# Optimization experiments

Hardware: AMD Instinct MI355X
Metric: run time of the kernel (lower is better)

## Reference

```python
import jax, jax.numpy as jnp
import numpy as np

EMBEDDING_DIM = 64  # matches init_kwargs; temperature = sqrt(embedding_dim)


def setup_inputs() -> dict:
    key = jax.random.key(0)
    k1, k2, k3, k4 = jax.random.split(key, 4)
    B, S, D = 8, 2048, EMBEDDING_DIM
    return {
        "key": jax.random.normal(k1, (B, S, D), dtype=jnp.float32),
        "query": jax.random.normal(k2, (B, S, D), dtype=jnp.float32),
        "value": jax.random.normal(k3, (B, S, D), dtype=jnp.float32),
        "query_attention_mask": jax.random.randint(k4, (B, S), 0, 2, dtype=jnp.int32),
    }


def reference(key, query, value, query_attention_mask):
    # scores: [B, S, S]
    temperature = jnp.sqrt(jnp.asarray(EMBEDDING_DIM, dtype=query.dtype))
    scores = jnp.einsum("bqd,bkd->bqk", query, key) / temperature
    # masked_fill_ fills -inf WHERE mask is True (as in the torch source).
    # mask [B, S] -> broadcast over the query axis to [B, 1, S] -> [B, S, S].
    mask = query_attention_mask.astype(bool)[:, None, :]
    scores = jnp.where(mask, -jnp.inf, scores)
    attention_filter = jax.nn.softmax(scores, axis=-1)
    # dropout p=0.0 (deterministic reference) -> identity
    context = jnp.einsum("bqk,bkd->bqd", attention_filter, value)
    return (context, attention_filter)
```

## Files before the change

### kernel.cpp

```cpp
#include <hip/hip_runtime.h>
#include <hip/hip_bf16.h>
#include <math.h>


typedef short bf16x8 __attribute__((ext_vector_type(8)));
typedef short bf16x4 __attribute__((ext_vector_type(4)));
typedef float f32x4 __attribute__((ext_vector_type(4)));

#define BATCH 8
#define SDIM 2048
#define DDIM 64
#define KBLK 64
#define NBLK (SDIM / KBLK)
#define KSPLIT 4
#define BPW (NBLK / KSPLIT)
#define NROWS (BATCH * SDIM)
#define SCALE 0.125f
#define KSTR 72

__device__ __forceinline__ short f2bf(float f) {
    unsigned x = __float_as_uint(f);
    x = (x + 0x7fffu + ((x >> 16) & 1u)) >> 16;
    return (short)x;
}
__device__ __forceinline__ float fidx(const float4& v, int i) {
    return ((const float*)&v)[i];
}

__global__ __launch_bounds__(256, 4)
void attn_prep(const float* __restrict__ Kg, const float* __restrict__ Vg,
               short* __restrict__ Kbf, short* __restrict__ VTbf,
               float* __restrict__ Ctx)
{
    __shared__ short VTlds[DDIM][KSTR];

    const int wg = blockIdx.x;
    const int b = wg & 7;
    const int kbase = (wg >> 3) * KBLK;
    const int tid = threadIdx.x;

    const float* Kb = Kg + (size_t)b * SDIM * DDIM;
    const float* Vb = Vg + (size_t)b * SDIM * DDIM;

    {
        const int key = tid >> 2, doff = (tid & 3) * 16;
        const float* src = Kb + (size_t)(kbase + key) * DDIM + doff;
        float4 f0 = *(const float4*)(src);
        float4 f1 = *(const float4*)(src + 4);
        float4 f2 = *(const float4*)(src + 8);
        float4 f3 = *(const float4*)(src + 12);
        bf16x8 p0, p1;
        p0[0]=f2bf(f0.x); p0[1]=f2bf(f0.y); p0[2]=f2bf(f0.z); p0[3]=f2bf(f0.w);
        p0[4]=f2bf(f1.x); p0[5]=f2bf(f1.y); p0[6]=f2bf(f1.z); p0[7]=f2bf(f1.w);
        p1[0]=f2bf(f2.x); p1[1]=f2bf(f2.y); p1[2]=f2bf(f2.z); p1[3]=f2bf(f2.w);
        p1[4]=f2bf(f3.x); p1[5]=f2bf(f3.y); p1[6]=f2bf(f3.z); p1[7]=f2bf(f3.w);
        short* dst = Kbf + ((size_t)b * SDIM + kbase + key) * DDIM + doff;
        *(bf16x8*)dst = p0;
        *(bf16x8*)(dst + 8) = p1;
    }

    {
        const int sv_d0 = (tid & 15) * 4, sv_k0 = (tid >> 4) * 4;
        float4 vreg[4];
        #pragma unroll
        for (int i = 0; i < 4; ++i)
            vreg[i] = *(const float4*)(Vb + (size_t)(kbase + sv_k0 + i) * DDIM + sv_d0);
        #pragma unroll
        for (int dd = 0; dd < 4; ++dd) {
            bf16x4 pv;
            pv[0] = f2bf(fidx(vreg[0], dd));
            pv[1] = f2bf(fidx(vreg[1], dd));
            pv[2] = f2bf(fidx(vreg[2], dd));
            pv[3] = f2bf(fidx(vreg[3], dd));
            *(bf16x4*)&VTlds[sv_d0 + dd][sv_k0] = pv;
        }
    }
    __syncthreads();
    {
        const int d = tid >> 2, koff = (tid & 3) * 16;
        bf16x8 a = *(const bf16x8*)&VTlds[d][koff];
        bf16x8 c = *(const bf16x8*)&VTlds[d][koff + 8];
        short* dst = VTbf + ((size_t)b * DDIM + d) * SDIM + kbase + koff;
        *(bf16x8*)dst = a;
        *(bf16x8*)(dst + 8) = c;
    }

    {
        float4* dst = (float4*)Ctx + (size_t)wg * 1024;
        for (int i = tid; i < 1024; i += 256) dst[i] = make_float4(0.f, 0.f, 0.f, 0.f);
    }
}

__global__ __launch_bounds__(256, 4)
void attn_stats(const short* __restrict__ Kbf, const float* __restrict__ Qg,
                const int* __restrict__ Mg, float* __restrict__ part)
{
    __shared__ short Klds[KBLK][KSTR];
    __shared__ int   Mlds[KBLK];

    const int wg = blockIdx.x;
    const int b = wg & 7;
    const int qt = (wg >> 3) & 31;
    const int sp = wg >> 8;
    const int tid = threadIdx.x;
    const int w = tid >> 6, lane = tid & 63, col = lane & 15, quad = lane >> 4;

    const float* Qb = Qg + (size_t)b * SDIM * DDIM;
    const int*   Mb = Mg + (size_t)b * SDIM;

    bf16x8 aq[2];
    {
        const float* qsrc = Qb + (size_t)(qt * 64 + w * 16 + col) * DDIM + quad * 8;
        #pragma unroll
        for (int c = 0; c < 2; ++c) {
            float4 f0 = *(const float4*)(qsrc + c * 32);
            float4 f1 = *(const float4*)(qsrc + c * 32 + 4);
            bf16x8 a;
            a[0]=f2bf(f0.x); a[1]=f2bf(f0.y); a[2]=f2bf(f0.z); a[3]=f2bf(f0.w);
            a[4]=f2bf(f1.x); a[5]=f2bf(f1.y); a[6]=f2bf(f1.z); a[7]=f2bf(f1.w);
            aq[c] = a;
        }
    }

    const int skey = tid >> 2;
    const int sdoff = (tid & 3) * 16;
    const int kb0 = sp * BPW * KBLK;
    const short* Ksp = Kbf + ((size_t)b * SDIM + kb0) * DDIM;

    float lsum[4];
    #pragma unroll
    for (int r = 0; r < 4; ++r) lsum[r] = 0.0f;

    bf16x8 ks0, ks1;
    int mreg = 0;
    {
        const short* src = Ksp + (size_t)skey * DDIM + sdoff;
        ks0 = *(const bf16x8*)src;
        ks1 = *(const bf16x8*)(src + 8);
        if (tid < KBLK) mreg = Mb[kb0 + tid];
    }

    for (int kb = 0; kb < BPW; ++kb) {
        __syncthreads();
        *(bf16x8*)&Klds[skey][sdoff]     = ks0;
        *(bf16x8*)&Klds[skey][sdoff + 8] = ks1;
        if (tid < KBLK) Mlds[tid] = mreg;
        __syncthreads();
        if (kb + 1 < BPW) {
            const short* src = Ksp + (size_t)((kb + 1) * KBLK + skey) * DDIM + sdoff;
            ks0 = *(const bf16x8*)src;
            ks1 = *(const bf16x8*)(src + 8);
            if (tid < KBLK) mreg = Mb[kb0 + (kb + 1) * KBLK + tid];
        }

        #pragma unroll
        for (int t = 0; t < 4; ++t) {
            f32x4 acc = {0.f, 0.f, 0.f, 0.f};
            #pragma unroll
            for (int c = 0; c < 2; ++c) {
                bf16x8 bk = *(const bf16x8*)&Klds[t * 16 + col][c * 32 + quad * 8];
                acc = __builtin_amdgcn_mfma_f32_16x16x32_bf16(aq[c], bk, acc, 0, 0, 0);
            }
            const int mk = Mlds[t * 16 + col];
            #pragma unroll
            for (int r = 0; r < 4; ++r)
                lsum[r] += mk ? 0.0f : __expf(acc[r] * SCALE);
        }
    }

    #pragma unroll
    for (int r = 0; r < 4; ++r) {
        float s = lsum[r];
        s += __shfl_xor(s, 1);
        s += __shfl_xor(s, 2);
        s += __shfl_xor(s, 4);
        s += __shfl_xor(s, 8);
        lsum[r] = s;
    }
    if (col == 0) {
        #pragma unroll
        for (int r = 0; r < 4; ++r)
            part[(size_t)sp * NROWS + b * SDIM + qt * 64 + w * 16 + quad * 4 + r] = lsum[r];
    }
}

__global__ __launch_bounds__(256)
void attn_merge(const float* __restrict__ part, float* __restrict__ stats)
{
    const int t = blockIdx.x * 256 + threadIdx.x;
    if (t < NROWS) {
        float l = part[t] + part[NROWS + t] + part[2 * NROWS + t] + part[3 * NROWS + t];
        stats[t] = 1.0f / l;
    }
}

__global__ __launch_bounds__(256, 4)
void attn_emit(const short* __restrict__ Kbf, const short* __restrict__ VTbf,
               const float* __restrict__ Qg, const int* __restrict__ Mg,
               const float* __restrict__ stats, float* __restrict__ Ctx,
               float* __restrict__ Filt)
{
    __shared__ short Klds[KBLK][KSTR];
    __shared__ short VTlds[DDIM][KSTR];
    __shared__ short Plds[4][16][KSTR];
    __shared__ int   Mlds[KBLK];

    const int wg = blockIdx.x;
    const int b = wg & 7;
    const int qt = (wg >> 3) & 31;
    const int sp = wg >> 8;
    const int tid = threadIdx.x;
    const int w = tid >> 6, lane = tid & 63, col = lane & 15, quad = lane >> 4;

    const float* Qb = Qg + (size_t)b * SDIM * DDIM;
    const int*   Mb = Mg + (size_t)b * SDIM;
    float* Ctxb  = Ctx  + (size_t)b * SDIM * DDIM;
    float* Filtb = Filt + (size_t)b * SDIM * SDIM;

    bf16x8 aq[2];
    {
        const float* qsrc = Qb + (size_t)(qt * 64 + w * 16 + col) * DDIM + quad * 8;
        #pragma unroll
        for (int c = 0; c < 2; ++c) {
            float4 f0 = *(const float4*)(qsrc + c * 32);
            float4 f1 = *(const float4*)(qsrc + c * 32 + 4);
            bf16x8 a;
            a[0]=f2bf(f0.x); a[1]=f2bf(f0.y); a[2]=f2bf(f0.z); a[3]=f2bf(f0.w);
            a[4]=f2bf(f1.x); a[5]=f2bf(f1.y); a[6]=f2bf(f1.z); a[7]=f2bf(f1.w);
            aq[c] = a;
        }
    }

    float invl[4];
    #pragma unroll
    for (int r = 0; r < 4; ++r)
        invl[r] = stats[b * SDIM + qt * 64 + w * 16 + quad * 4 + r];

    const int skey = tid >> 2;
    const int sdoff = (tid & 3) * 16;
    const int kb0 = sp * BPW * KBLK;
    const short* Ksp = Kbf + ((size_t)b * SDIM + kb0) * DDIM;
    const short* VTb = VTbf + (size_t)b * DDIM * SDIM;
    const int vd = tid >> 2, vkoff = (tid & 3) * 16;

    f32x4 Oacc[4];
    #pragma unroll
    for (int dt = 0; dt < 4; ++dt) Oacc[dt] = (f32x4){0.f, 0.f, 0.f, 0.f};

    bf16x8 ks0, ks1, vt0, vt1;
    int mreg = 0;
    {
        const short* srck = Ksp + (size_t)skey * DDIM + sdoff;
        ks0 = *(const bf16x8*)srck;
        ks1 = *(const bf16x8*)(srck + 8);
        const short* srcv = VTb + (size_t)vd * SDIM + kb0 + vkoff;
        vt0 = *(const bf16x8*)srcv;
        vt1 = *(const bf16x8*)(srcv + 8);
        if (tid < KBLK) mreg = Mb[kb0 + tid];
    }

    for (int kb = 0; kb < BPW; ++kb) {
        const int kbase = kb0 + kb * KBLK;
        __syncthreads();
        *(bf16x8*)&Klds[skey][sdoff]      = ks0;
        *(bf16x8*)&Klds[skey][sdoff + 8]  = ks1;
        *(bf16x8*)&VTlds[vd][vkoff]       = vt0;
        *(bf16x8*)&VTlds[vd][vkoff + 8]   = vt1;
        if (tid < KBLK) Mlds[tid] = mreg;
        __syncthreads();
        if (kb + 1 < BPW) {
            const short* srck = Ksp + (size_t)((kb + 1) * KBLK + skey) * DDIM + sdoff;
            ks0 = *(const bf16x8*)srck;
            ks1 = *(const bf16x8*)(srck + 8);
            const short* srcv = VTb + (size_t)vd * SDIM + (kbase + KBLK) + vkoff;
            vt0 = *(const bf16x8*)srcv;
            vt1 = *(const bf16x8*)(srcv + 8);
            if (tid < KBLK) mreg = Mb[kbase + KBLK + tid];
        }

        #pragma unroll
        for (int t = 0; t < 4; ++t) {
            f32x4 acc = {0.f, 0.f, 0.f, 0.f};
            #pragma unroll
            for (int c = 0; c < 2; ++c) {
                bf16x8 bk = *(const bf16x8*)&Klds[t * 16 + col][c * 32 + quad * 8];
                acc = __builtin_amdgcn_mfma_f32_16x16x32_bf16(aq[c], bk, acc, 0, 0, 0);
            }
            const int mk = Mlds[t * 16 + col];
            #pragma unroll
            for (int r = 0; r < 4; ++r) {
                float p = mk ? 0.0f : __expf(acc[r] * SCALE) * invl[r];
                __builtin_nontemporal_store(
                    p, &Filtb[(size_t)(qt * 64 + w * 16 + quad * 4 + r) * SDIM + kbase + t * 16 + col]);
                Plds[w][quad * 4 + r][t * 16 + col] = f2bf(p);
            }
        }

        #pragma unroll
        for (int c = 0; c < 2; ++c) {
            bf16x8 ap = *(const bf16x8*)&Plds[w][col][c * 32 + quad * 8];
            #pragma unroll
            for (int dt = 0; dt < 4; ++dt) {
                bf16x8 bv = *(const bf16x8*)&VTlds[dt * 16 + col][c * 32 + quad * 8];
                Oacc[dt] = __builtin_amdgcn_mfma_f32_16x16x32_bf16(ap, bv, Oacc[dt], 0, 0, 0);
            }
        }
    }

    #pragma unroll
    for (int dt = 0; dt < 4; ++dt) {
        #pragma unroll
        for (int r = 0; r < 4; ++r) {
            unsafeAtomicAdd(&Ctxb[(size_t)(qt * 64 + w * 16 + quad * 4 + r) * DDIM + dt * 16 + col],
                            Oacc[dt][r]);
        }
    }
}

extern "C" void kernel_launch(void* const* d_in, const int* in_sizes, int n_in,
                              void* d_out, int out_size, void* d_ws, size_t ws_size,
                              hipStream_t stream) {
    const float* Kg = (const float*)d_in[0];
    const float* Qg = (const float*)d_in[1];
    const float* Vg = (const float*)d_in[2];
    const int*   Mg = (const int*)d_in[3];
    float* Ctx  = (float*)d_out;
    float* Filt = (float*)d_out + (size_t)BATCH * SDIM * DDIM;

    short* Kbf  = (short*)d_ws;
    short* VTbf = Kbf + (size_t)BATCH * SDIM * DDIM;
    float* part  = (float*)(VTbf + (size_t)BATCH * DDIM * SDIM);
    float* stats = part + (size_t)KSPLIT * NROWS;

    attn_prep<<<dim3(BATCH * NBLK), dim3(256), 0, stream>>>(Kg, Vg, Kbf, VTbf, Ctx);
    attn_stats<<<dim3(BATCH * NBLK * KSPLIT), dim3(256), 0, stream>>>(Kbf, Qg, Mg, part);
    attn_merge<<<dim3(NROWS / 256), dim3(256), 0, stream>>>(part, stats);
    attn_emit<<<dim3(BATCH * NBLK * KSPLIT), dim3(256), 0, stream>>>(Kbf, VTbf, Qg, Mg, stats, Ctx, Filt);
}
```

Baseline: 187.9 us.

## Drop LDS staging, swap MFMA operands for row-contiguous stores, replace atomics with partial reduce

K, V^T and mask fragments are now loaded straight from global memory into registers, double-buffered in registers, instead of being staged through LDS with barriers. The MFMA operands are swapped so each lane holds four consecutive keys of one query row, which lets the attention-filter writes become 16-byte vector stores and the mask reads int4 loads. The scale is folded into Q before the bf16 conversion. The merge kernel is folded into emit. The context atomics and zero-fill are replaced by per-split partial outputs summed in a new reduction kernel. The changes add register pressure and an extra workspace write and read, and redundant global loads across waves replace shared LDS reuse.

Result: slower. 291.5 us (+55.2%).

```diff
diff --git a/kernel.cpp b/kernel.cpp
--- a/kernel.cpp
+++ b/kernel.cpp
@@ -1,5 +1,4 @@
 #include <hip/hip_runtime.h>
-#include <hip/hip_bf16.h>
 #include <math.h>
 
 
@@ -29,8 +28,7 @@
 
 __global__ __launch_bounds__(256, 4)
 void attn_prep(const float* __restrict__ Kg, const float* __restrict__ Vg,
-               short* __restrict__ Kbf, short* __restrict__ VTbf,
-               float* __restrict__ Ctx)
+               short* __restrict__ Kbf, short* __restrict__ VTbf)
 {
     __shared__ short VTlds[DDIM][KSTR];
 
@@ -84,20 +82,12 @@
         *(bf16x8*)dst = a;
         *(bf16x8*)(dst + 8) = c;
     }
-
-    {
-        float4* dst = (float4*)Ctx + (size_t)wg * 1024;
-        for (int i = tid; i < 1024; i += 256) dst[i] = make_float4(0.f, 0.f, 0.f, 0.f);
-    }
 }
 
 __global__ __launch_bounds__(256, 4)
 void attn_stats(const short* __restrict__ Kbf, const float* __restrict__ Qg,
                 const int* __restrict__ Mg, float* __restrict__ part)
 {
-    __shared__ short Klds[KBLK][KSTR];
-    __shared__ int   Mlds[KBLK];
-
     const int wg = blockIdx.x;
     const int b = wg & 7;
     const int qt = (wg >> 3) & 31;
@@ -105,105 +95,60 @@
     const int tid = threadIdx.x;
     const int w = tid >> 6, lane = tid & 63, col = lane & 15, quad = lane >> 4;
 
-    const float* Qb = Qg + (size_t)b * SDIM * DDIM;
-    const int*   Mb = Mg + (size_t)b * SDIM;
-
     bf16x8 aq[2];
     {
-        const float* qsrc = Qb + (size_t)(qt * 64 + w * 16 + col) * DDIM + quad * 8;
+        const float* qsrc = Qg + ((size_t)b * SDIM + qt * 64 + w * 16 + col) * DDIM + quad * 8;
         #pragma unroll
         for (int c = 0; c < 2; ++c) {
             float4 f0 = *(const float4*)(qsrc + c * 32);
             float4 f1 = *(const float4*)(qsrc + c * 32 + 4);
             bf16x8 a;
-            a[0]=f2bf(f0.x); a[1]=f2bf(f0.y); a[2]=f2bf(f0.z); a[3]=f2bf(f0.w);
-            a[4]=f2bf(f1.x); a[5]=f2bf(f1.y); a[6]=f2bf(f1.z); a[7]=f2bf(f1.w);
+            a[0]=f2bf(f0.x*SCALE); a[1]=f2bf(f0.y*SCALE); a[2]=f2bf(f0.z*SCALE); a[3]=f2bf(f0.w*SCALE);
+            a[4]=f2bf(f1.x*SCALE); a[5]=f2bf(f1.y*SCALE); a[6]=f2bf(f1.z*SCALE); a[7]=f2bf(f1.w*SCALE);
             aq[c] = a;
         }
     }
 
-    const int skey = tid >> 2;
-    const int sdoff = (tid & 3) * 16;
     const int kb0 = sp * BPW * KBLK;
-    const short* Ksp = Kbf + ((size_t)b * SDIM + kb0) * DDIM;
-
-    float lsum[4];
-    #pragma unroll
-    for (int r = 0; r < 4; ++r) lsum[r] = 0.0f;
-
-    bf16x8 ks0, ks1;
-    int mreg = 0;
-    {
-        const short* src = Ksp + (size_t)skey * DDIM + sdoff;
-        ks0 = *(const bf16x8*)src;
-        ks1 = *(const bf16x8*)(src + 8);
-        if (tid < KBLK) mreg = Mb[kb0 + tid];
-    }
-
+    const short* Kb = Kbf + (size_t)b * SDIM * DDIM;
+    const int*   Mb = Mg + (size_t)b * SDIM;
+
+    float lsum = 0.0f;
     for (int kb = 0; kb < BPW; ++kb) {
-        __syncthreads();
-        *(bf16x8*)&Klds[skey][sdoff]     = ks0;
-        *(bf16x8*)&Klds[skey][sdoff + 8] = ks1;
-        if (tid < KBLK) Mlds[tid] = mreg;
-        __syncthreads();
-        if (kb + 1 < BPW) {
-            const short* src = Ksp + (size_t)((kb + 1) * KBLK + skey) * DDIM + sdoff;
-            ks0 = *(const bf16x8*)src;
-            ks1 = *(const bf16x8*)(src + 8);
-            if (tid < KBLK) mreg = Mb[kb0 + (kb + 1) * KBLK + tid];
-        }
-
+        const int kbase = kb0 + kb * KBLK;
+        bf16x8 kf[4][2];
+        #pragma unroll
+        for (int t = 0; t < 4; ++t) {
+            const short* ks = Kb + (size_t)(kbase + t * 16 + col) * DDIM + quad * 8;
+            kf[t][0] = *(const bf16x8*)ks;
+            kf[t][1] = *(const bf16x8*)(ks + 32);
+        }
         #pragma unroll
         for (int t = 0; t < 4; ++t) {
             f32x4 acc = {0.f, 0.f, 0.f, 0.f};
-            #pragma unroll
-            for (int c = 0; c < 2; ++c) {
-                bf16x8 bk = *(const bf16x8*)&Klds[t * 16 + col][c * 32 + quad * 8];
-                acc = __builtin_amdgcn_mfma_f32_16x16x32_bf16(aq[c], bk, acc, 0, 0, 0);
-            }
-            const int mk = Mlds[t * 16 + col];
-            #pragma unroll
-            for (int r = 0; r < 4; ++r)
-                lsum[r] += mk ? 0.0f : __expf(acc[r] * SCALE);
-        }
-    }
-
-    #pragma unroll
-    for (int r = 0; r < 4; ++r) {
-        float s = lsum[r];
-        s += __shfl_xor(s, 1);
-        s += __shfl_xor(s, 2);
-        s += __shfl_xor(s, 4);
-        s += __shfl_xor(s, 8);
-        lsum[r] = s;
-    }
-    if (col == 0) {
-        #pragma unroll
-        for (int r = 0; r < 4; ++r)
-            part[(size_t)sp * NROWS + b * SDIM + qt * 64 + w * 16 + quad * 4 + r] = lsum[r];
-    }
-}
-
-__global__ __launch_bounds__(256)
-void attn_merge(const float* __restrict__ part, float* __restrict__ stats)
-{
-    const int t = blockIdx.x * 256 + threadIdx.x;
-    if (t < NROWS) {
-        float l = part[t] + part[NROWS + t] + part[2 * NROWS + t] + part[3 * NROWS + t];
-        stats[t] = 1.0f / l;
-    }
+            acc = __builtin_amdgcn_mfma_f32_16x16x32_bf16(kf[t][0], aq[0], acc, 0, 0, 0);
+            acc = __builtin_amdgcn_mfma_f32_16x16x32_bf16(kf[t][1], aq[1], acc, 0, 0, 0);
+            int4 mq = *(const int4*)(Mb + kbase + t * 16 + quad * 4);
+            lsum += mq.x ? 0.0f : __expf(acc[0]);
+            lsum += mq.y ? 0.0f : __expf(acc[1]);
+            lsum += mq.z ? 0.0f : __expf(acc[2]);
+            lsum += mq.w ? 0.0f : __expf(acc[3]);
+        }
+    }
+
+    lsum += __shfl_xor(lsum, 16);
+    lsum += __shfl_xor(lsum, 32);
+    if (quad == 0)
+        part[(size_t)sp * NROWS + (size_t)b * SDIM + qt * 64 + w * 16 + col] = lsum;
 }
 
 __global__ __launch_bounds__(256, 4)
 void attn_emit(const short* __restrict__ Kbf, const short* __restrict__ VTbf,
                const float* __restrict__ Qg, const int* __restrict__ Mg,
-               const float* __restrict__ stats, float* __restrict__ Ctx,
+               const float* __restrict__ part, float* __restrict__ Opart,
                float* __restrict__ Filt)
 {
-    __shared__ short Klds[KBLK][KSTR];
-    __shared__ short VTlds[DDIM][KSTR];
     __shared__ short Plds[4][16][KSTR];
-    __shared__ int   Mlds[KBLK];
 
     const int wg = blockIdx.x;
     const int b = wg & 7;
@@ -212,109 +157,135 @@
     const int tid = threadIdx.x;
     const int w = tid >> 6, lane = tid & 63, col = lane & 15, quad = lane >> 4;
 
-    const float* Qb = Qg + (size_t)b * SDIM * DDIM;
     const int*   Mb = Mg + (size_t)b * SDIM;
-    float* Ctxb  = Ctx  + (size_t)b * SDIM * DDIM;
+    const short* Kb = Kbf + (size_t)b * SDIM * DDIM;
+    const short* VTb = VTbf + (size_t)b * DDIM * SDIM;
     float* Filtb = Filt + (size_t)b * SDIM * SDIM;
 
     bf16x8 aq[2];
     {
-        const float* qsrc = Qb + (size_t)(qt * 64 + w * 16 + col) * DDIM + quad * 8;
+        const float* qsrc = Qg + ((size_t)b * SDIM + qt * 64 + w * 16 + col) * DDIM + quad * 8;
         #pragma unroll
         for (int c = 0; c < 2; ++c) {
             float4 f0 = *(const float4*)(qsrc + c * 32);
             float4 f1 = *(const float4*)(qsrc + c * 32 + 4);
             bf16x8 a;
-            a[0]=f2bf(f0.x); a[1]=f2bf(f0.y); a[2]=f2bf(f0.z); a[3]=f2bf(f0.w);
-            a[4]=f2bf(f1.x); a[5]=f2bf(f1.y); a[6]=f2bf(f1.z); a[7]=f2bf(f1.w);
+            a[0]=f2bf(f0.x*SCALE); a[1]=f2bf(f0.y*SCALE); a[2]=f2bf(f0.z*SCALE); a[3]=f2bf(f0.w*SCALE);
+            a[4]=f2bf(f1.x*SCALE); a[5]=f2bf(f1.y*SCALE); a[6]=f2bf(f1.z*SCALE); a[7]=f2bf(f1.w*SCALE);
             aq[c] = a;
         }
     }
 
-    float invl[4];
-    #pragma unroll
-    for (int r = 0; r < 4; ++r)
-        invl[r] = stats[b * SDIM + qt * 64 + w * 16 + quad * 4 + r];
-
-    const int skey = tid >> 2;
-    const int sdoff = (tid & 3) * 16;
+    float invl;
+    {
+        const size_t row = (size_t)b * SDIM + qt * 64 + w * 16 + col;
+        invl = 1.0f / (part[row] + part[NROWS + row] +
+                       part[2 * NROWS + row] + part[3 * NROWS + row]);
+    }
+
     const int kb0 = sp * BPW * KBLK;
-    const short* Ksp = Kbf + ((size_t)b * SDIM + kb0) * DDIM;
-    const short* VTb = VTbf + (size_t)b * DDIM * SDIM;
-    const int vd = tid >> 2, vkoff = (tid & 3) * 16;
 
     f32x4 Oacc[4];
     #pragma unroll
     for (int dt = 0; dt < 4; ++dt) Oacc[dt] = (f32x4){0.f, 0.f, 0.f, 0.f};
 
-    bf16x8 ks0, ks1, vt0, vt1;
-    int mreg = 0;
-    {
-        const short* srck = Ksp + (size_t)skey * DDIM + sdoff;
-        ks0 = *(const bf16x8*)srck;
-        ks1 = *(const bf16x8*)(srck + 8);
-        const short* srcv = VTb + (size_t)vd * SDIM + kb0 + vkoff;
-        vt0 = *(const bf16x8*)srcv;
-        vt1 = *(const bf16x8*)(srcv + 8);
-        if (tid < KBLK) mreg = Mb[kb0 + tid];
+    bf16x8 kfA[4][2], vtA[2][4];
+    int4 mqA[4];
+    {
+        #pragma unroll
+        for (int t = 0; t < 4; ++t) {
+            const short* ks = Kb + (size_t)(kb0 + t * 16 + col) * DDIM + quad * 8;
+            kfA[t][0] = *(const bf16x8*)ks;
+            kfA[t][1] = *(const bf16x8*)(ks + 32);
+        }
+        #pragma unroll
+        for (int c = 0; c < 2; ++c)
+            #pragma unroll
+            for (int dt = 0; dt < 4; ++dt)
+                vtA[c][dt] = *(const bf16x8*)(VTb + (size_t)(dt * 16 + col) * SDIM + kb0 + c * 32 + quad * 8);
+        #pragma unroll
+        for (int t = 0; t < 4; ++t)
+            mqA[t] = *(const int4*)(Mb + kb0 + t * 16 + quad * 4);
     }
 
     for (int kb = 0; kb < BPW; ++kb) {
         const int kbase = kb0 + kb * KBLK;
-        __syncthreads();
-        *(bf16x8*)&Klds[skey][sdoff]      = ks0;
-        *(bf16x8*)&Klds[skey][sdoff + 8]  = ks1;
-        *(bf16x8*)&VTlds[vd][vkoff]       = vt0;
-        *(bf16x8*)&VTlds[vd][vkoff + 8]   = vt1;
-        if (tid < KBLK) Mlds[tid] = mreg;
-        __syncthreads();
-        if (kb + 1 < BPW) {
-            const short* srck = Ksp + (size_t)((kb + 1) * KBLK + skey) * DDIM + sdoff;
-            ks0 = *(const bf16x8*)srck;
-            ks1 = *(const bf16x8*)(srck + 8);
-            const short* srcv = VTb + (size_t)vd * SDIM + (kbase + KBLK) + vkoff;
-            vt0 = *(const bf16x8*)srcv;
-            vt1 = *(const bf16x8*)(srcv + 8);
-            if (tid < KBLK) mreg = Mb[kbase + KBLK + tid];
+
+        bf16x8 kfB[4][2], vtB[2][4];
+        int4 mqB[4];
+        const bool has_next = (kb + 1 < BPW);
+        if (has_next) {
+            const int kn = kbase + KBLK;
+            #pragma unroll
+            for (int t = 0; t < 4; ++t) {
+                const short* ks = Kb + (size_t)(kn + t * 16 + col) * DDIM + quad * 8;
+                kfB[t][0] = *(const bf16x8*)ks;
+                kfB[t][1] = *(const bf16x8*)(ks + 32);
+            }
+            #pragma unroll
+            for (int c = 0; c < 2; ++c)
+                #pragma unroll
+                for (int dt = 0; dt < 4; ++dt)
+                    vtB[c][dt] = *(const bf16x8*)(VTb + (size_t)(dt * 16 + col) * SDIM + kn + c * 32 + quad * 8);
+            #pragma unroll
+            for (int t = 0; t < 4; ++t)
+                mqB[t] = *(const int4*)(Mb + kn + t * 16 + quad * 4);
         }
 
         #pragma unroll
         for (int t = 0; t < 4; ++t) {
             f32x4 acc = {0.f, 0.f, 0.f, 0.f};
-            #pragma unroll
-            for (int c = 0; c < 2; ++c) {
-                bf16x8 bk = *(const bf16x8*)&Klds[t * 16 + col][c * 32 + quad * 8];
-                acc = __builtin_amdgcn_mfma_f32_16x16x32_bf16(aq[c], bk, acc, 0, 0, 0);
-            }
-            const int mk = Mlds[t * 16 + col];
-            #pragma unroll
-            for (int r = 0; r < 4; ++r) {
-                float p = mk ? 0.0f : __expf(acc[r] * SCALE) * invl[r];
-                __builtin_nontemporal_store(
-                    p, &Filtb[(size_t)(qt * 64 + w * 16 + quad * 4 + r) * SDIM + kbase + t * 16 + col]);
-                Plds[w][quad * 4 + r][t * 16 + col] = f2bf(p);
-            }
+            acc = __builtin_amdgcn_mfma_f32_16x16x32_bf16(kfA[t][0], aq[0], acc, 0, 0, 0);
+            acc = __builtin_amdgcn_mfma_f32_16x16x32_bf16(kfA[t][1], aq[1], acc, 0, 0, 0);
+            f32x4 p4;
+            p4[0] = mqA[t].x ? 0.0f : __expf(acc[0]) * invl;
+            p4[1] = mqA[t].y ? 0.0f : __expf(acc[1]) * invl;
+            p4[2] = mqA[t].z ? 0.0f : __expf(acc[2]) * invl;
+            p4[3] = mqA[t].w ? 0.0f : __expf(acc[3]) * invl;
+            f32x4* fdst = (f32x4*)&Filtb[(size_t)(qt * 64 + w * 16 + col) * SDIM + kbase + t * 16 + quad * 4];
+            __builtin_nontemporal_store(p4, fdst);
+            bf16x4 pb;
+            pb[0] = f2bf(p4[0]); pb[1] = f2bf(p4[1]);
+            pb[2] = f2bf(p4[2]); pb[3] = f2bf(p4[3]);
+            *(bf16x4*)&Plds[w][col][t * 16 + quad * 4] = pb;
         }
 
         #pragma unroll
         for (int c = 0; c < 2; ++c) {
             bf16x8 ap = *(const bf16x8*)&Plds[w][col][c * 32 + quad * 8];
             #pragma unroll
-            for (int dt = 0; dt < 4; ++dt) {
-                bf16x8 bv = *(const bf16x8*)&VTlds[dt * 16 + col][c * 32 + quad * 8];
-                Oacc[dt] = __builtin_amdgcn_mfma_f32_16x16x32_bf16(ap, bv, Oacc[dt], 0, 0, 0);
-            }
-        }
-    }
-
+            for (int dt = 0; dt < 4; ++dt)
+                Oacc[dt] = __builtin_amdgcn_mfma_f32_16x16x32_bf16(ap, vtA[c][dt], Oacc[dt], 0, 0, 0);
+        }
+
+        if (has_next) {
+            #pragma unroll
+            for (int t = 0; t < 4; ++t) { kfA[t][0] = kfB[t][0]; kfA[t][1] = kfB[t][1]; mqA[t] = mqB[t]; }
+            #pragma unroll
+            for (int c = 0; c < 2; ++c)
+                #pragma unroll
+                for (int dt = 0; dt < 4; ++dt) vtA[c][dt] = vtB[c][dt];
+        }
+    }
+
+    float* Ob = Opart + ((size_t)sp * NROWS + (size_t)b * SDIM) * DDIM;
     #pragma unroll
     for (int dt = 0; dt < 4; ++dt) {
         #pragma unroll
-        for (int r = 0; r < 4; ++r) {
-            unsafeAtomicAdd(&Ctxb[(size_t)(qt * 64 + w * 16 + quad * 4 + r) * DDIM + dt * 16 + col],
-                            Oacc[dt][r]);
-        }
-    }
+        for (int r = 0; r < 4; ++r)
+            Ob[(size_t)(qt * 64 + w * 16 + quad * 4 + r) * DDIM + dt * 16 + col] = Oacc[dt][r];
+    }
+}
+
+__global__ __launch_bounds__(256)
+void attn_ctx(const float* __restrict__ Opart, float* __restrict__ Ctx)
+{
+    const size_t t = (size_t)blockIdx.x * 256 + threadIdx.x;
+    const size_t Qn = (size_t)NROWS * DDIM / 4;
+    const f32x4* op = (const f32x4*)Opart;
+    f32x4 s0 = op[t] + op[Qn + t];
+    f32x4 s1 = op[2 * Qn + t] + op[3 * Qn + t];
+    ((f32x4*)Ctx)[t] = s0 + s1;
 }
 
 extern "C" void kernel_launch(void* const* d_in, const int* in_sizes, int n_in,
@@ -329,11 +300,11 @@
 
     short* Kbf  = (short*)d_ws;
     short* VTbf = Kbf + (size_t)BATCH * SDIM * DDIM;
-    float* part  = (float*)(VTbf + (size_t)BATCH * DDIM * SDIM);
-    float* stats = part + (size_t)KSPLIT * NROWS;
-
-    attn_prep<<<dim3(BATCH * NBLK), dim3(256), 0, stream>>>(Kg, Vg, Kbf, VTbf, Ctx);
+    float* part = (float*)(VTbf + (size_t)BATCH * DDIM * SDIM);
+    float* Opart = part + (size_t)KSPLIT * NROWS;
+
+    attn_prep<<<dim3(BATCH * NBLK), dim3(256), 0, stream>>>(Kg, Vg, Kbf, VTbf);
     attn_stats<<<dim3(BATCH * NBLK * KSPLIT), dim3(256), 0, stream>>>(Kbf, Qg, Mg, part);
-    attn_merge<<<dim3(NROWS / 256), dim3(256), 0, stream>>>(part, stats);
-    attn_emit<<<dim3(BATCH * NBLK * KSPLIT), dim3(256), 0, stream>>>(Kbf, VTbf, Qg, Mg, stats, Ctx, Filt);
-}
+    attn_emit<<<dim3(BATCH * NBLK * KSPLIT), dim3(256), 0, stream>>>(Kbf, VTbf, Qg, Mg, part, Opart, Filt);
+    attn_ctx<<<dim3(NROWS * DDIM / 4 / 256), dim3(256), 0, stream>>>(Opart, Ctx);
+}
```
